# Performance work log

Hardware: AMD Instinct MI355X
Metric: run time of the kernel (lower is better)

The kernel has to match this reference:

```python
import jax, jax.numpy as jnp
import numpy as np

B, INDIM, OUTDIM = 1024, 2048, 4096


def setup_inputs() -> dict:
    key = jax.random.key(0)
    kx, kw, kb = jax.random.split(key, 3)
    x = jax.random.normal(kx, (B, INDIM), dtype=jnp.float32)
    # nn.Linear(indim, outdim): weight [outdim, indim], bias [outdim]
    bound = 1.0 / np.sqrt(INDIM)
    W = jax.random.uniform(kw, (OUTDIM, INDIM), minval=-bound, maxval=bound, dtype=jnp.float32)
    b = jax.random.uniform(kb, (OUTDIM,), minval=-bound, maxval=bound, dtype=jnp.float32)
    return {"x": x, "W": W, "b": b}


def reference(x, W, b):
    # Faithful to torch: prototypes = weight.transpose(0,1).reshape(outdim, indim)
    # (a reflatten of W^T, not the original weight rows, since outdim != indim).
    protos = W.T.reshape(W.shape[0], W.shape[1])  # [outdim, indim]
    # -||x_i - p_j||^2 - b_j via GEMM identity (same math as broadcast subtract + norm^2)
    x_sq = jnp.sum(x * x, axis=1, keepdims=True)          # [B, 1]
    p_sq = jnp.sum(protos * protos, axis=1)[None, :]      # [1, outdim]
    xp = jnp.einsum('bd,od->bo', x, protos)               # [B, outdim]
    return -(x_sq - 2.0 * xp + p_sq) - b[None, :]
```

## Files before the change

### kernel.cpp

```cpp
#include <hip/hip_runtime.h>

#define B_DIM   1024
#define IN_DIM  2048
#define OUT_DIM 4096

typedef __bf16 bf16x8 __attribute__((ext_vector_type(8)));
typedef float  f32x4  __attribute__((ext_vector_type(4)));
typedef unsigned short u16x8 __attribute__((ext_vector_type(8)));

__device__ __forceinline__ unsigned short f2bf(float f) {
    union { float f; unsigned int u; } cv; cv.f = f;
    unsigned int u = cv.u;
    unsigned int r = 0x7fffu + ((u >> 16) & 1u);
    return (unsigned short)((u + r) >> 16);
}

__device__ __forceinline__ float bf2f(unsigned short h) {
    union { unsigned int u; float f; } cv; cv.u = ((unsigned int)h) << 16;
    return cv.f;
}

__device__ __forceinline__ void async16(const void* g, void* l) {
    __builtin_amdgcn_global_load_lds(
        (const __attribute__((address_space(1))) unsigned int*)g,
        (__attribute__((address_space(3))) unsigned int*)l,
        16, 0, 0);
}

extern "C" __global__ __launch_bounds__(256) void transpose_w(
        const float* __restrict__ W, unsigned short* __restrict__ protos) {
    __shared__ float tile[64][65];
    const int r  = blockIdx.z;
    const int c0 = blockIdx.x * 64;
    const int d0 = blockIdx.y * 64;
    const int t  = threadIdx.x;
    const int g  = t >> 4;
    const int cc = (t & 15) * 4;

    const float* Wp = W + (size_t)(r * IN_DIM + d0 + g) * IN_DIM + c0 + cc;
#pragma unroll
    for (int p = 0; p < 4; ++p) {
        const float4 v = *(const float4*)(Wp + (size_t)(16 * p) * IN_DIM);
        const int dl = g + 16 * p;
        tile[dl][cc]     = v.x;
        tile[dl][cc + 1] = v.y;
        tile[dl][cc + 2] = v.z;
        tile[dl][cc + 3] = v.w;
    }
    __syncthreads();

#pragma unroll
    for (int p = 0; p < 4; ++p) {
        const int cr = g + 16 * p;
        const int o  = 2 * (c0 + cr) + r;
        ushort4 pk;
        pk.x = f2bf(tile[cc][cr]);
        pk.y = f2bf(tile[cc + 1][cr]);
        pk.z = f2bf(tile[cc + 2][cr]);
        pk.w = f2bf(tile[cc + 3][cr]);
        *(ushort4*)(protos + (size_t)o * IN_DIM + d0 + cc) = pk;
    }
}

extern "C" __global__ __launch_bounds__(256) void psq_bias(
        const unsigned short* __restrict__ protos,
        const float* __restrict__ bias,
        float* __restrict__ psb) {
    const int o    = blockIdx.x * 4 + (threadIdx.x >> 6);
    const int lane = threadIdx.x & 63;
    const unsigned short* p = protos + (size_t)o * IN_DIM + lane * 8;
    float s = 0.f;
#pragma unroll
    for (int it = 0; it < 4; ++it) {
        u16x8 v = *(const u16x8*)(p + it * 512);
#pragma unroll
        for (int e = 0; e < 8; ++e) {
            const float f = bf2f(v[e]);
            s += f * f;
        }
    }
#pragma unroll
    for (int off = 32; off > 0; off >>= 1) s += __shfl_down(s, off);
    if (lane == 0) psb[o] = s + bias[o];
}

extern "C" __global__ __launch_bounds__(256) void xcast_xsq(
        const float* __restrict__ x,
        unsigned short* __restrict__ xb,
        float* __restrict__ x_sq) {
    __shared__ float red[4];
    const int b = blockIdx.x;
    const int t = threadIdx.x;
    const float* xp = x + (size_t)b * IN_DIM + t * 8;
    const float4 v0 = ((const float4*)xp)[0];
    const float4 v1 = ((const float4*)xp)[1];
    u16x8 pk;
    pk[0] = f2bf(v0.x); pk[1] = f2bf(v0.y); pk[2] = f2bf(v0.z); pk[3] = f2bf(v0.w);
    pk[4] = f2bf(v1.x); pk[5] = f2bf(v1.y); pk[6] = f2bf(v1.z); pk[7] = f2bf(v1.w);
    *(u16x8*)(xb + (size_t)b * IN_DIM + t * 8) = pk;

    float s = v0.x * v0.x + v0.y * v0.y + v0.z * v0.z + v0.w * v0.w
            + v1.x * v1.x + v1.y * v1.y + v1.z * v1.z + v1.w * v1.w;
#pragma unroll
    for (int off = 32; off > 0; off >>= 1) s += __shfl_down(s, off);
    const int lane = t & 63, w = t >> 6;
    if (lane == 0) red[w] = s;
    __syncthreads();
    if (t == 0) x_sq[b] = red[0] + red[1] + red[2] + red[3];
}

extern "C" __global__ __launch_bounds__(256) void gemm_epi(
        const unsigned short* __restrict__ A,
        const unsigned short* __restrict__ Bt,
        const float* __restrict__ x_sq,
        const float* __restrict__ psb,
        float* __restrict__ out) {
    __shared__ __align__(16) unsigned short lA[64 * 64];
    __shared__ __align__(16) unsigned short lB[64 * 64];

    const int lid = blockIdx.x;
    const int xcd = lid & 7;
    const int wi  = lid >> 3;
    const int nt  = xcd * 8 + (wi & 7);
    const int mt  = wi >> 3;
    const int m0 = mt * 64;
    const int n0 = nt * 64;

    const int t = threadIdx.x;
    const int rA = t >> 3;
    const int gc = (t & 7) ^ (rA & 7);
    const unsigned short* gA0 = A  + (size_t)(m0 + rA) * IN_DIM + gc * 8;
    const unsigned short* gA1 = gA0 + (size_t)32 * IN_DIM;
    const unsigned short* gB0 = Bt + (size_t)(n0 + rA) * IN_DIM + gc * 8;
    const unsigned short* gB1 = gB0 + (size_t)32 * IN_DIM;
    unsigned short* lA0 = lA + t * 8;
    unsigned short* lA1 = lA0 + 2048;
    unsigned short* lB0 = lB + t * 8;
    unsigned short* lB1 = lB0 + 2048;

    const int wave = t >> 6;
    const int lane = t & 63;
    const int wm = (wave & 1) * 32;
    const int wn = (wave >> 1) * 32;
    const int ln = lane & 15;
    const int qd = lane >> 4;
    const int sw = ln & 7;

    f32x4 acc[2][2] = {};

    for (int k0 = 0; k0 < IN_DIM; k0 += 64) {
        async16(gA0, lA0); async16(gA1, lA1);
        async16(gB0, lB0); async16(gB1, lB1);
        gA0 += 64; gA1 += 64; gB0 += 64; gB1 += 64;
        __syncthreads();

        bf16x8 af[2][2], bfr[2][2];
#pragma unroll
        for (int i = 0; i < 2; ++i)
#pragma unroll
            for (int kk = 0; kk < 2; ++kk) {
                const int pcA = (kk * 4 + qd) ^ sw;
                af[i][kk]  = *(const bf16x8*)(lA + (wm + i * 16 + ln) * 64 + pcA * 8);
                bfr[i][kk] = *(const bf16x8*)(lB + (wn + i * 16 + ln) * 64 + pcA * 8);
            }
#pragma unroll
        for (int kk = 0; kk < 2; ++kk)
#pragma unroll
            for (int i = 0; i < 2; ++i)
#pragma unroll
                for (int j = 0; j < 2; ++j)
                    acc[i][j] = __builtin_amdgcn_mfma_f32_16x16x32_bf16(
                                    af[i][kk], bfr[j][kk], acc[i][j], 0, 0, 0);
        __syncthreads();
    }

    const int rowb = m0 + wm;
    const int colb = n0 + wn;
#pragma unroll
    for (int j = 0; j < 2; ++j) {
        const int col = colb + j * 16 + ln;
        const float pb = psb[col];
#pragma unroll
        for (int i = 0; i < 2; ++i) {
            const int row0 = rowb + i * 16 + qd * 4;
#pragma unroll
            for (int rr = 0; rr < 4; ++rr) {
                const int row = row0 + rr;
                out[(size_t)row * OUT_DIM + col] = 2.0f * acc[i][j][rr] - x_sq[row] - pb;
            }
        }
    }
}

extern "C" void kernel_launch(void* const* d_in, const int* in_sizes, int n_in,
                              void* d_out, int out_size, void* d_ws, size_t ws_size,
                              hipStream_t stream) {
    const float* x    = (const float*)d_in[0];
    const float* W    = (const float*)d_in[1];
    const float* bias = (const float*)d_in[2];
    float* out = (float*)d_out;

    char* ws = (char*)d_ws;
    unsigned short* protos = (unsigned short*)ws;
    unsigned short* xb     = (unsigned short*)(ws + (size_t)16 * 1024 * 1024);
    float* x_sq            = (float*)(ws + (size_t)20 * 1024 * 1024);
    float* psb             = (float*)(ws + (size_t)20 * 1024 * 1024 + 8192);

    transpose_w<<<dim3(32, 32, 2), 256, 0, stream>>>(W, protos);
    psq_bias<<<dim3(1024), 256, 0, stream>>>(protos, bias, psb);
    xcast_xsq<<<dim3(1024), 256, 0, stream>>>(x, xb, x_sq);
    gemm_epi<<<dim3(1024), 256, 0, stream>>>(xb, protos, x_sq, psb, out);
}
```

Baseline: 117.6 us.

## Switch GEMM operands to FP8 and fuse prototype norms into transpose

New measurement: 109.7 us. 6.8% less time.

```diff
diff --git a/kernel.cpp b/kernel.cpp
--- a/kernel.cpp
+++ b/kernel.cpp
@@ -1,23 +1,15 @@
 #include <hip/hip_runtime.h>
 
-#define B_DIM   1024
 #define IN_DIM  2048
 #define OUT_DIM 4096
 
-typedef __bf16 bf16x8 __attribute__((ext_vector_type(8)));
-typedef float  f32x4  __attribute__((ext_vector_type(4)));
-typedef unsigned short u16x8 __attribute__((ext_vector_type(8)));
+typedef float     f32x4 __attribute__((ext_vector_type(4)));
+typedef long long llx2  __attribute__((ext_vector_type(2)));
 
-__device__ __forceinline__ unsigned short f2bf(float f) {
-    union { float f; unsigned int u; } cv; cv.f = f;
-    unsigned int u = cv.u;
-    unsigned int r = 0x7fffu + ((u >> 16) & 1u);
-    return (unsigned short)((u + r) >> 16);
-}
-
-__device__ __forceinline__ float bf2f(unsigned short h) {
-    union { unsigned int u; float f; } cv; cv.u = ((unsigned int)h) << 16;
-    return cv.f;
+__device__ __forceinline__ unsigned int pk4(float a, float b, float c, float d) {
+    int v = __builtin_amdgcn_cvt_pk_fp8_f32(a, b, 0, false);
+    v     = __builtin_amdgcn_cvt_pk_fp8_f32(c, d, v, true);
+    return (unsigned int)v;
 }
 
 __device__ __forceinline__ void async16(const void* g, void* l) {
@@ -27,8 +19,11 @@
         16, 0, 0);
 }
 
+__device__ __forceinline__ int gmem_of(int c) { return 2 * (c & 3) + (c >> 2); }
+
 extern "C" __global__ __launch_bounds__(256) void transpose_w(
-        const float* __restrict__ W, unsigned short* __restrict__ protos) {
+        const float* __restrict__ W, unsigned char* __restrict__ protos,
+        float* __restrict__ psq) {
     __shared__ float tile[64][65];
     const int r  = blockIdx.z;
     const int c0 = blockIdx.x * 64;
@@ -49,44 +44,33 @@
     }
     __syncthreads();
 
+    const int c8 = t & 7;
+    const int gm = gmem_of(c8);
 #pragma unroll
-    for (int p = 0; p < 4; ++p) {
-        const int cr = g + 16 * p;
-        const int o  = 2 * (c0 + cr) + r;
-        ushort4 pk;
-        pk.x = f2bf(tile[cc][cr]);
-        pk.y = f2bf(tile[cc + 1][cr]);
-        pk.z = f2bf(tile[cc + 2][cr]);
-        pk.w = f2bf(tile[cc + 3][cr]);
-        *(ushort4*)(protos + (size_t)o * IN_DIM + d0 + cc) = pk;
+    for (int p = 0; p < 2; ++p) {
+        const int cr = (t >> 3) + 32 * p;
+        float v[8];
+        float ss = 0.f;
+#pragma unroll
+        for (int j = 0; j < 8; ++j) {
+            v[j] = tile[8 * c8 + j][cr];
+            ss += v[j] * v[j];
+        }
+        const int o = 2 * (c0 + cr) + r;
+        uint2 pk;
+        pk.x = pk4(16.f * v[0], 16.f * v[1], 16.f * v[2], 16.f * v[3]);
+        pk.y = pk4(16.f * v[4], 16.f * v[5], 16.f * v[6], 16.f * v[7]);
+        *(uint2*)(protos + (size_t)o * IN_DIM + d0 + gm * 8) = pk;
+        ss += __shfl_xor(ss, 1);
+        ss += __shfl_xor(ss, 2);
+        ss += __shfl_xor(ss, 4);
+        if (c8 == 0) atomicAdd(psq + o, ss);
     }
-}
-
-extern "C" __global__ __launch_bounds__(256) void psq_bias(
-        const unsigned short* __restrict__ protos,
-        const float* __restrict__ bias,
-        float* __restrict__ psb) {
-    const int o    = blockIdx.x * 4 + (threadIdx.x >> 6);
-    const int lane = threadIdx.x & 63;
-    const unsigned short* p = protos + (size_t)o * IN_DIM + lane * 8;
-    float s = 0.f;
-#pragma unroll
-    for (int it = 0; it < 4; ++it) {
-        u16x8 v = *(const u16x8*)(p + it * 512);
-#pragma unroll
-        for (int e = 0; e < 8; ++e) {
-            const float f = bf2f(v[e]);
-            s += f * f;
-        }
-    }
-#pragma unroll
-    for (int off = 32; off > 0; off >>= 1) s += __shfl_down(s, off);
-    if (lane == 0) psb[o] = s + bias[o];
 }
 
 extern "C" __global__ __launch_bounds__(256) void xcast_xsq(
         const float* __restrict__ x,
-        unsigned short* __restrict__ xb,
+        unsigned char* __restrict__ xb,
         float* __restrict__ x_sq) {
     __shared__ float red[4];
     const int b = blockIdx.x;
@@ -94,10 +78,10 @@
     const float* xp = x + (size_t)b * IN_DIM + t * 8;
     const float4 v0 = ((const float4*)xp)[0];
     const float4 v1 = ((const float4*)xp)[1];
-    u16x8 pk;
-    pk[0] = f2bf(v0.x); pk[1] = f2bf(v0.y); pk[2] = f2bf(v0.z); pk[3] = f2bf(v0.w);
-    pk[4] = f2bf(v1.x); pk[5] = f2bf(v1.y); pk[6] = f2bf(v1.z); pk[7] = f2bf(v1.w);
-    *(u16x8*)(xb + (size_t)b * IN_DIM + t * 8) = pk;
+    uint2 pk;
+    pk.x = pk4(v0.x, v0.y, v0.z, v0.w);
+    pk.y = pk4(v1.x, v1.y, v1.z, v1.w);
+    *(uint2*)(xb + (size_t)b * IN_DIM + (t >> 3) * 64 + gmem_of(t & 7) * 8) = pk;
 
     float s = v0.x * v0.x + v0.y * v0.y + v0.z * v0.z + v0.w * v0.w
             + v1.x * v1.x + v1.y * v1.y + v1.z * v1.z + v1.w * v1.w;
@@ -110,13 +94,14 @@
 }
 
 extern "C" __global__ __launch_bounds__(256) void gemm_epi(
-        const unsigned short* __restrict__ A,
-        const unsigned short* __restrict__ Bt,
+        const unsigned char* __restrict__ A,
+        const unsigned char* __restrict__ Bt,
         const float* __restrict__ x_sq,
-        const float* __restrict__ psb,
+        const float* __restrict__ psq,
+        const float* __restrict__ bias,
         float* __restrict__ out) {
-    __shared__ __align__(16) unsigned short lA[64 * 64];
-    __shared__ __align__(16) unsigned short lB[64 * 64];
+    __shared__ __align__(16) unsigned char lA[64 * 64];
+    __shared__ __align__(16) unsigned char lB[64 * 64];
 
     const int lid = blockIdx.x;
     const int xcd = lid & 7;
@@ -126,17 +111,13 @@
     const int m0 = mt * 64;
     const int n0 = nt * 64;
 
-    const int t = threadIdx.x;
-    const int rA = t >> 3;
-    const int gc = (t & 7) ^ (rA & 7);
-    const unsigned short* gA0 = A  + (size_t)(m0 + rA) * IN_DIM + gc * 8;
-    const unsigned short* gA1 = gA0 + (size_t)32 * IN_DIM;
-    const unsigned short* gB0 = Bt + (size_t)(n0 + rA) * IN_DIM + gc * 8;
-    const unsigned short* gB1 = gB0 + (size_t)32 * IN_DIM;
-    unsigned short* lA0 = lA + t * 8;
-    unsigned short* lA1 = lA0 + 2048;
-    unsigned short* lB0 = lB + t * 8;
-    unsigned short* lB1 = lB0 + 2048;
+    const int t  = threadIdx.x;
+    const int rS = t >> 2;
+    const int pS = (t & 3) ^ ((rS >> 1) & 3);
+    const unsigned char* gA = A  + (size_t)(m0 + rS) * IN_DIM + pS * 16;
+    const unsigned char* gB = Bt + (size_t)(n0 + rS) * IN_DIM + pS * 16;
+    unsigned char* lAd = lA + t * 16;
+    unsigned char* lBd = lB + t * 16;
 
     const int wave = t >> 6;
     const int lane = t & 63;
@@ -144,33 +125,31 @@
     const int wn = (wave >> 1) * 32;
     const int ln = lane & 15;
     const int qd = lane >> 4;
-    const int sw = ln & 7;
+    const int pf = qd ^ ((ln >> 1) & 3);
 
     f32x4 acc[2][2] = {};
 
     for (int k0 = 0; k0 < IN_DIM; k0 += 64) {
-        async16(gA0, lA0); async16(gA1, lA1);
-        async16(gB0, lB0); async16(gB1, lB1);
-        gA0 += 64; gA1 += 64; gB0 += 64; gB1 += 64;
+        async16(gA, lAd);
+        async16(gB, lBd);
+        gA += 64; gB += 64;
         __syncthreads();
 
-        bf16x8 af[2][2], bfr[2][2];
+        llx2 af[2], bf[2];
 #pragma unroll
         for (int i = 0; i < 2; ++i)
+            af[i] = *(const llx2*)(lA + (wm + i * 16 + ln) * 64 + pf * 16);
 #pragma unroll
-            for (int kk = 0; kk < 2; ++kk) {
-                const int pcA = (kk * 4 + qd) ^ sw;
-                af[i][kk]  = *(const bf16x8*)(lA + (wm + i * 16 + ln) * 64 + pcA * 8);
-                bfr[i][kk] = *(const bf16x8*)(lB + (wn + i * 16 + ln) * 64 + pcA * 8);
-            }
+        for (int j = 0; j < 2; ++j)
+            bf[j] = *(const llx2*)(lB + (wn + j * 16 + ln) * 64 + pf * 16);
 #pragma unroll
         for (int kk = 0; kk < 2; ++kk)
 #pragma unroll
             for (int i = 0; i < 2; ++i)
 #pragma unroll
                 for (int j = 0; j < 2; ++j)
-                    acc[i][j] = __builtin_amdgcn_mfma_f32_16x16x32_bf16(
-                                    af[i][kk], bfr[j][kk], acc[i][j], 0, 0, 0);
+                    acc[i][j] = __builtin_amdgcn_mfma_f32_16x16x32_fp8_fp8(
+                                    af[i][kk], bf[j][kk], acc[i][j], 0, 0, 0);
         __syncthreads();
     }
 
@@ -179,14 +158,15 @@
 #pragma unroll
     for (int j = 0; j < 2; ++j) {
         const int col = colb + j * 16 + ln;
-        const float pb = psb[col];
+        const float pb = psq[col] + bias[col];
 #pragma unroll
         for (int i = 0; i < 2; ++i) {
             const int row0 = rowb + i * 16 + qd * 4;
 #pragma unroll
             for (int rr = 0; rr < 4; ++rr) {
                 const int row = row0 + rr;
-                out[(size_t)row * OUT_DIM + col] = 2.0f * acc[i][j][rr] - x_sq[row] - pb;
+                out[(size_t)row * OUT_DIM + col] =
+                    0.125f * acc[i][j][rr] - x_sq[row] - pb;
             }
         }
     }
@@ -201,13 +181,13 @@
     float* out = (float*)d_out;
 
     char* ws = (char*)d_ws;
-    unsigned short* protos = (unsigned short*)ws;
-    unsigned short* xb     = (unsigned short*)(ws + (size_t)16 * 1024 * 1024);
-    float* x_sq            = (float*)(ws + (size_t)20 * 1024 * 1024);
-    float* psb             = (float*)(ws + (size_t)20 * 1024 * 1024 + 8192);
+    unsigned char* protos = (unsigned char*)ws;
+    unsigned char* xb     = (unsigned char*)(ws + (size_t)8 * 1024 * 1024);
+    float* x_sq           = (float*)(ws + (size_t)10 * 1024 * 1024);
+    float* psq            = (float*)(ws + (size_t)10 * 1024 * 1024 + 8192);
 
-    transpose_w<<<dim3(32, 32, 2), 256, 0, stream>>>(W, protos);
-    psq_bias<<<dim3(1024), 256, 0, stream>>>(protos, bias, psb);
+    hipMemsetAsync(psq, 0, OUT_DIM * sizeof(float), stream);
+    transpose_w<<<dim3(32, 32, 2), 256, 0, stream>>>(W, protos, psq);
     xcast_xsq<<<dim3(1024), 256, 0, stream>>>(x, xb, x_sq);
-    gemm_epi<<<dim3(1024), 256, 0, stream>>>(xb, protos, x_sq, psb, out);
+    gemm_epi<<<dim3(1024), 256, 0, stream>>>(xb, protos, x_sq, psq, bias, out);
 }
```
